# Kernel tuning notes

Hardware: AMD Instinct MI355X
Metric: run time of the kernel (lower is better)

The kernel has to match this reference:

```python
import jax, jax.numpy as jnp
import numpy as np

EMBED = 512
HEADS = 8
HEAD_DIM = EMBED // HEADS


def setup_inputs() -> dict:
    key = jax.random.key(0)
    ks = jax.random.split(key, 12)
    B, L, D = 2, 4096, EMBED
    s = 1.0 / np.sqrt(D)  # torch Linear default init range scale (approx, uniform)
    def lin(k):
        kw, kb = jax.random.split(k)
        W = jax.random.uniform(kw, (D, D), jnp.float32, -s, s)
        b = jax.random.uniform(kb, (D,), jnp.float32, -s, s)
        return W, b
    Wq, bq = lin(ks[0])
    Wk, bk = lin(ks[1])
    Wv, bv = lin(ks[2])
    Wo, bo = lin(ks[3])
    query = jax.random.normal(ks[4], (B, L, D), jnp.float32)
    key_t = jax.random.normal(ks[5], (B, L, D), jnp.float32)
    value = jax.random.normal(ks[6], (B, L, D), jnp.float32)
    return {"query": query, "key": key_t, "value": value,
            "Wq": Wq, "bq": bq, "Wk": Wk, "bk": bk,
            "Wv": Wv, "bv": bv, "Wo": Wo, "bo": bo}


def reference(query, key, value, Wq, bq, Wk, bk, Wv, bv, Wo, bo):
    B, L, D = query.shape
    H, Hd = HEADS, HEAD_DIM
    scale = Hd ** -0.5
    # torch nn.Linear: y = x @ W.T + b
    q = (query @ Wq.T + bq).reshape(B, L, H, Hd).transpose(0, 2, 1, 3)   # [B,H,L,Hd]
    k = (key   @ Wk.T + bk).reshape(B, -1, H, Hd).transpose(0, 2, 1, 3)
    v = (value @ Wv.T + bv).reshape(B, -1, H, Hd).transpose(0, 2, 1, 3)
    scores = jnp.einsum('bhqd,bhkd->bhqk', q, k) * scale                  # [B,H,L,L]
    causal = jnp.triu(jnp.ones((L, L), dtype=bool), k=1)                  # True above diag
    neg = jnp.finfo(scores.dtype).min
    scores = jnp.where(causal, neg, scores)
    attn = jax.nn.softmax(scores, axis=-1)
    # dropout is identity in eval mode
    out = jnp.einsum('bhqk,bhkd->bhqd', attn, v)                          # [B,H,L,Hd]
    out = out.transpose(0, 2, 1, 3).reshape(B, L, D)
    return out @ Wo.T + bo, attn
```

## Files before the change

kernel.cpp:

```cpp
#include <hip/hip_runtime.h>
#include <hip/hip_bf16.h>


typedef __attribute__((ext_vector_type(8))) __bf16 bf16x8;
typedef __attribute__((ext_vector_type(4))) __bf16 bf16v4;
typedef __attribute__((ext_vector_type(4))) float f32x4;

constexpr int LL = 4096;
constexpr int DD = 512;
constexpr int HH = 8;
constexpr int HD = 64;
constexpr int BB = 2;
constexpr int BL = BB * LL;
constexpr size_t OUT_ELEMS = (size_t)BB * LL * DD;
constexpr int CH = 16;
constexpr int NCHUNK = LL / 64 / CH;

static __device__ inline bf16x8 cvt8(const float* p) {
    float4 a = *reinterpret_cast<const float4*>(p);
    float4 b = *reinterpret_cast<const float4*>(p + 4);
    bf16x8 r;
    r[0] = (__bf16)a.x; r[1] = (__bf16)a.y; r[2] = (__bf16)a.z; r[3] = (__bf16)a.w;
    r[4] = (__bf16)b.x; r[5] = (__bf16)b.y; r[6] = (__bf16)b.z; r[7] = (__bf16)b.w;
    return r;
}

__global__ __launch_bounds__(256) void cvt_kernel(
    const float* __restrict__ q, const float* __restrict__ k,
    const float* __restrict__ v, __bf16* __restrict__ o)
{
    constexpr size_t N = (size_t)BL * DD;
    size_t i = ((size_t)blockIdx.x * 256 + threadIdx.x) * 8;
    const float* src = q; size_t j = i;
    if (i >= 2 * N)      { src = v; j = i - 2 * N; }
    else if (i >= N)     { src = k; j = i - N; }
    *reinterpret_cast<bf16x8*>(&o[i]) = cvt8(&src[j]);
}

__global__ __launch_bounds__(256) void qkv_kernel(
    const __bf16* __restrict__ Xb,
    const float* __restrict__ Wq, const float* __restrict__ bq,
    const float* __restrict__ Wk, const float* __restrict__ bk,
    const float* __restrict__ Wv, const float* __restrict__ bv,
    __bf16* __restrict__ Qb, __bf16* __restrict__ Kb, __bf16* __restrict__ Vt)
{
    const int z = blockIdx.z;
    const __bf16* x  = Xb + (size_t)z * BL * DD;
    const float* W   = (z == 0) ? Wq : (z == 1) ? Wk : Wv;
    const float* bia = (z == 0) ? bq : (z == 1) ? bk : bv;

    const int wid = threadIdx.x >> 6;
    const int lane = threadIdx.x & 63;
    const int l15 = lane & 15;
    const int lg  = lane >> 4;

    const int r0 = blockIdx.x * 64;
    const int cb = blockIdx.y;
    const int c0 = cb * 64 + wid * 16;

    f32x4 acc[4] = {};
    for (int k0 = 0; k0 < DD; k0 += 32) {
        bf16x8 bfrag = cvt8(&W[(size_t)(c0 + l15) * DD + k0 + lg * 8]);
#pragma unroll
        for (int mt = 0; mt < 4; ++mt) {
            bf16x8 afrag = *reinterpret_cast<const bf16x8*>(
                &x[(size_t)(r0 + mt * 16 + l15) * DD + k0 + lg * 8]);
            acc[mt] = __builtin_amdgcn_mfma_f32_16x16x32_bf16(afrag, bfrag, acc[mt], 0, 0, 0);
        }
    }

    __shared__ __bf16 T[64][72];
    const float bval = bia[c0 + l15];
#pragma unroll
    for (int mt = 0; mt < 4; ++mt)
#pragma unroll
        for (int i = 0; i < 4; ++i) {
            const float val = acc[mt][i] + bval;
            const int row = mt * 16 + lg * 4 + i;
            const int col = wid * 16 + l15;
            if (z == 2) T[col][row] = (__bf16)val;
            else        T[row][col] = (__bf16)val;
        }
    __syncthreads();

    const int tr  = threadIdx.x >> 2;
    const int seg = threadIdx.x & 3;
    uint4 v0 = *reinterpret_cast<const uint4*>(&T[tr][seg * 16]);
    uint4 v1 = *reinterpret_cast<const uint4*>(&T[tr][seg * 16 + 8]);
    const int b  = r0 >> 12;
    const int l0 = r0 & (LL - 1);
    if (z == 2) {
        __bf16* dst = Vt + ((size_t)(b * HH + cb) * HD + tr) * LL + l0 + seg * 16;
        *reinterpret_cast<uint4*>(dst)     = v0;
        *reinterpret_cast<uint4*>(dst + 8) = v1;
    } else {
        __bf16* base = (z == 0) ? Qb : Kb;
        __bf16* dst = base + ((size_t)(b * HH + cb) * LL + l0 + tr) * HD + seg * 16;
        *reinterpret_cast<uint4*>(dst)     = v0;
        *reinterpret_cast<uint4*>(dst + 8) = v1;
    }
}

__global__ __launch_bounds__(256) void rowsum_kernel(
    const __bf16* __restrict__ Qb, const __bf16* __restrict__ Kb,
    float* __restrict__ rspart)
{
    const int bh = blockIdx.x;
    const int qb = 63 - blockIdx.y;
    const int ch = blockIdx.z;
    if (ch * CH > qb) return;

    const int wv   = threadIdx.x >> 6;
    const int lane = threadIdx.x & 63;
    const int l15  = lane & 15;
    const int lg   = lane >> 4;

    const __bf16* Qh = Qb + (size_t)bh * LL * HD;
    const __bf16* Kh = Kb + (size_t)bh * LL * HD;

    const int q0 = qb * 64 + wv * 16;
    const int qrow = q0 + l15;
    const bf16x8 qf0 = *reinterpret_cast<const bf16x8*>(&Qh[(size_t)qrow * HD + lg * 8]);
    const bf16x8 qf1 = *reinterpret_cast<const bf16x8*>(&Qh[(size_t)qrow * HD + 32 + lg * 8]);
    const float SC = 0.125f * 1.44269504088896f;

    float rs = 0.f;
    const int kend = (qb < ch * CH + CH - 1) ? qb : ch * CH + CH - 1;
    for (int kb = ch * CH; kb <= kend; ++kb) {
        f32x4 s[4] = {};
#pragma unroll
        for (int kt = 0; kt < 4; ++kt) {
            const __bf16* kp = &Kh[(size_t)(kb * 64 + kt * 16 + l15) * HD + lg * 8];
            const bf16x8 k0 = *reinterpret_cast<const bf16x8*>(kp);
            const bf16x8 k1 = *reinterpret_cast<const bf16x8*>(kp + 32);
            s[kt] = __builtin_amdgcn_mfma_f32_16x16x32_bf16(k0, qf0, s[kt], 0, 0, 0);
            s[kt] = __builtin_amdgcn_mfma_f32_16x16x32_bf16(k1, qf1, s[kt], 0, 0, 0);
        }
        const bool diag = (kb == qb);
#pragma unroll
        for (int kt = 0; kt < 4; ++kt)
#pragma unroll
            for (int i = 0; i < 4; ++i) {
                float e = exp2f(s[kt][i] * SC);
                if (diag && (kb * 64 + kt * 16 + lg * 4 + i) > qrow) e = 0.f;
                rs += e;
            }
    }
    rs += __shfl_xor(rs, 16, 64);
    rs += __shfl_xor(rs, 32, 64);
    if (lane < 16)
        rspart[((size_t)bh * LL + qrow) * NCHUNK + ch] = rs;
}

__global__ __launch_bounds__(256, 4) void attn_main_kernel(
    const __bf16* __restrict__ Qb, const __bf16* __restrict__ Kb,
    const __bf16* __restrict__ Vt, const float* __restrict__ rspart,
    __bf16* __restrict__ opart, float* __restrict__ attn_out)
{
    const int bh = blockIdx.x;
    const int qb = 63 - blockIdx.y;
    const int ch = blockIdx.z;

    const int wv   = threadIdx.x >> 6;
    const int lane = threadIdx.x & 63;
    const int l15  = lane & 15;
    const int lg   = lane >> 4;

    float* A_out = attn_out + (size_t)bh * LL * LL;
    const int q0 = qb * 64 + wv * 16;
    const int qrow = q0 + l15;
    const int kb0 = ch * CH;

    if (kb0 > qb) {
        const float4 z4 = {0.f, 0.f, 0.f, 0.f};
        float4* dst = reinterpret_cast<float4*>(&A_out[(size_t)qrow * LL + kb0 * 64 + lg * 4]);
        for (int t = 0; t < CH; ++t) {
#pragma unroll
            for (int kt = 0; kt < 4; ++kt) dst[kt * 4] = z4;
            dst += 16;
        }
        return;
    }

    const __bf16* Qh = Qb + (size_t)bh * LL * HD;
    const __bf16* Kh = Kb + (size_t)bh * LL * HD;
    const __bf16* Vh = Vt + (size_t)bh * HD * LL;

    __shared__ __bf16 P[4][16][72];

    const bf16x8 qf0 = *reinterpret_cast<const bf16x8*>(&Qh[(size_t)qrow * HD + lg * 8]);
    const bf16x8 qf1 = *reinterpret_cast<const bf16x8*>(&Qh[(size_t)qrow * HD + 32 + lg * 8]);

    float rsv = 0.f;
    const int nc = qb >> 4;
    const float* rp = &rspart[((size_t)bh * LL + qrow) * NCHUNK];
    for (int c = 0; c <= nc; ++c) rsv += rp[c];
    const float llog = -log2f(rsv);
    const float SC = 0.125f * 1.44269504088896f;

    f32x4 oacc[4] = {};

    for (int t = 0; t < CH; ++t) {
        const int kb = kb0 + t;
        if (kb > qb) {
            const float4 z4 = {0.f, 0.f, 0.f, 0.f};
            float4* dst = reinterpret_cast<float4*>(
                &A_out[(size_t)qrow * LL + kb * 64 + lg * 4]);
#pragma unroll
            for (int kt = 0; kt < 4; ++kt) dst[kt * 4] = z4;
            continue;
        }
        bf16x8 kf[8], vf[8];
        {
            const __bf16* kp = &Kh[(size_t)(kb * 64 + l15) * HD + lg * 8];
#pragma unroll
            for (int kt = 0; kt < 4; ++kt) {
                kf[kt * 2]     = *reinterpret_cast<const bf16x8*>(kp + (size_t)kt * 16 * HD);
                kf[kt * 2 + 1] = *reinterpret_cast<const bf16x8*>(kp + (size_t)kt * 16 * HD + 32);
            }
            const __bf16* vp = &Vh[(size_t)l15 * LL + (size_t)kb * 64 + lg * 8];
#pragma unroll
            for (int ht = 0; ht < 4; ++ht) {
                vf[ht * 2]     = *reinterpret_cast<const bf16x8*>(vp + (size_t)ht * 16 * LL);
                vf[ht * 2 + 1] = *reinterpret_cast<const bf16x8*>(vp + (size_t)ht * 16 * LL + 32);
            }
        }
        f32x4 s[4] = {};
#pragma unroll
        for (int kt = 0; kt < 4; ++kt) {
            s[kt] = __builtin_amdgcn_mfma_f32_16x16x32_bf16(kf[kt * 2],     qf0, s[kt], 0, 0, 0);
            s[kt] = __builtin_amdgcn_mfma_f32_16x16x32_bf16(kf[kt * 2 + 1], qf1, s[kt], 0, 0, 0);
        }
        const bool diag = (kb == qb);
#pragma unroll
        for (int kt = 0; kt < 4; ++kt) {
            float e0 = exp2f(fmaf(s[kt][0], SC, llog));
            float e1 = exp2f(fmaf(s[kt][1], SC, llog));
            float e2 = exp2f(fmaf(s[kt][2], SC, llog));
            float e3 = exp2f(fmaf(s[kt][3], SC, llog));
            if (diag) {
                const int kc = kb * 64 + kt * 16 + lg * 4;
                if (kc + 0 > qrow) e0 = 0.f;
                if (kc + 1 > qrow) e1 = 0.f;
                if (kc + 2 > qrow) e2 = 0.f;
                if (kc + 3 > qrow) e3 = 0.f;
            }
            float4 ev = {e0, e1, e2, e3};
            *reinterpret_cast<float4*>(
                &A_out[(size_t)qrow * LL + kb * 64 + kt * 16 + lg * 4]) = ev;
            bf16v4 pk;
            pk[0] = (__bf16)e0; pk[1] = (__bf16)e1;
            pk[2] = (__bf16)e2; pk[3] = (__bf16)e3;
            *reinterpret_cast<bf16v4*>(&P[wv][l15][kt * 16 + lg * 4]) = pk;
        }
        const bf16x8 pa0 = *reinterpret_cast<const bf16x8*>(&P[wv][l15][lg * 8]);
        const bf16x8 pa1 = *reinterpret_cast<const bf16x8*>(&P[wv][l15][32 + lg * 8]);
#pragma unroll
        for (int ht = 0; ht < 4; ++ht) {
            oacc[ht] = __builtin_amdgcn_mfma_f32_16x16x32_bf16(pa0, vf[ht * 2],     oacc[ht], 0, 0, 0);
            oacc[ht] = __builtin_amdgcn_mfma_f32_16x16x32_bf16(pa1, vf[ht * 2 + 1], oacc[ht], 0, 0, 0);
        }
    }

#pragma unroll
    for (int ht = 0; ht < 4; ++ht)
#pragma unroll
        for (int i = 0; i < 4; ++i)
            P[wv][lg * 4 + i][ht * 16 + l15] = (__bf16)oacc[ht][i];
    const int arow = lane >> 2;
    const int aseg = lane & 3;
    uint4 o0 = *reinterpret_cast<const uint4*>(&P[wv][arow][aseg * 16]);
    uint4 o1 = *reinterpret_cast<const uint4*>(&P[wv][arow][aseg * 16 + 8]);
    __bf16* dst = opart + ((size_t)((bh * 64 + qb) * NCHUNK + ch)) * 4096
                + (wv * 16 + arow) * 64 + aseg * 16;
    *reinterpret_cast<uint4*>(dst)     = o0;
    *reinterpret_cast<uint4*>(dst + 8) = o1;
}

__global__ __launch_bounds__(256) void oreduce_kernel(
    const __bf16* __restrict__ opart, __bf16* __restrict__ Ob)
{
    const int bh = blockIdx.x;
    const int qb = blockIdx.y;
    const int nc = qb >> 4;
    const __bf16* src = opart + ((size_t)(bh * 64 + qb) * NCHUNK) * 4096;
    const int t = threadIdx.x;

    float acc[16] = {};
    for (int c = 0; c <= nc; ++c) {
        bf16x8 a = *reinterpret_cast<const bf16x8*>(&src[(size_t)c * 4096 + t * 16]);
        bf16x8 b = *reinterpret_cast<const bf16x8*>(&src[(size_t)c * 4096 + t * 16 + 8]);
#pragma unroll
        for (int j = 0; j < 8; ++j) { acc[j] += (float)a[j]; acc[8 + j] += (float)b[j]; }
    }
    bf16x8 r0, r1;
#pragma unroll
    for (int j = 0; j < 8; ++j) { r0[j] = (__bf16)acc[j]; r1[j] = (__bf16)acc[8 + j]; }

    const int qr  = t >> 2;
    const int hd0 = (t & 3) * 16;
    const int b = bh >> 3, h = bh & 7;
    __bf16* dst = Ob + ((size_t)(b * LL + qb * 64 + qr)) * DD + h * HD + hd0;
    *reinterpret_cast<bf16x8*>(dst)     = r0;
    *reinterpret_cast<bf16x8*>(dst + 8) = r1;
}

__global__ __launch_bounds__(256) void oproj_kernel(
    const __bf16* __restrict__ Ob, const float* __restrict__ Wo,
    const float* __restrict__ bo, float* __restrict__ out)
{
    const int wid = threadIdx.x >> 6;
    const int lane = threadIdx.x & 63;
    const int l15 = lane & 15;
    const int lg  = lane >> 4;

    const int r0 = blockIdx.x * 64;
    const int c0 = blockIdx.y * 64 + wid * 16;

    f32x4 acc[4] = {};
    for (int k0 = 0; k0 < DD; k0 += 32) {
        bf16x8 bfrag = cvt8(&Wo[(size_t)(c0 + l15) * DD + k0 + lg * 8]);
#pragma unroll
        for (int mt = 0; mt < 4; ++mt) {
            bf16x8 afrag = *reinterpret_cast<const bf16x8*>(
                &Ob[(size_t)(r0 + mt * 16 + l15) * DD + k0 + lg * 8]);
            acc[mt] = __builtin_amdgcn_mfma_f32_16x16x32_bf16(afrag, bfrag, acc[mt], 0, 0, 0);
        }
    }
    const float bval = bo[c0 + l15];
#pragma unroll
    for (int mt = 0; mt < 4; ++mt)
#pragma unroll
        for (int i = 0; i < 4; ++i)
            out[(size_t)(r0 + mt * 16 + lg * 4 + i) * DD + c0 + l15] = acc[mt][i] + bval;
}

extern "C" void kernel_launch(void* const* d_in, const int* in_sizes, int n_in,
                              void* d_out, int out_size, void* d_ws, size_t ws_size,
                              hipStream_t stream) {
    const float* query = (const float*)d_in[0];
    const float* key_t = (const float*)d_in[1];
    const float* value = (const float*)d_in[2];
    const float* Wq = (const float*)d_in[3];
    const float* bq = (const float*)d_in[4];
    const float* Wk = (const float*)d_in[5];
    const float* bk = (const float*)d_in[6];
    const float* Wv = (const float*)d_in[7];
    const float* bv = (const float*)d_in[8];
    const float* Wo = (const float*)d_in[9];
    const float* bo = (const float*)d_in[10];

    float* out  = (float*)d_out;
    float* attn = out + OUT_ELEMS;

    char* ws = (char*)d_ws;
    __bf16* Qb     = (__bf16*)(ws);
    __bf16* Kb     = (__bf16*)(ws +  8388608);
    __bf16* Vt     = (__bf16*)(ws + 16777216);
    __bf16* Ob     = (__bf16*)(ws + 25165824);
    float*  rspart = (float*) (ws + 33554432);
    __bf16* Xb     = (__bf16*)(ws + 34603008);
    __bf16* opart  = (__bf16*)(ws + 34603008);

    cvt_kernel<<<dim3(3 * BL * DD / 8 / 256), 256, 0, stream>>>(query, key_t, value, Xb);
    qkv_kernel<<<dim3(BL / 64, DD / 64, 3), 256, 0, stream>>>(
        Xb, Wq, bq, Wk, bk, Wv, bv, Qb, Kb, Vt);
    rowsum_kernel<<<dim3(BB * HH, LL / 64, NCHUNK), 256, 0, stream>>>(Qb, Kb, rspart);
    attn_main_kernel<<<dim3(BB * HH, LL / 64, NCHUNK), 256, 0, stream>>>(
        Qb, Kb, Vt, rspart, opart, attn);
    oreduce_kernel<<<dim3(BB * HH, LL / 64), 256, 0, stream>>>(opart, Ob);
    oproj_kernel<<<dim3(BL / 64, DD / 64), 256, 0, stream>>>(Ob, Wo, bo, out);
}
```

Baseline: 786.8 us.

## Stage attention probs through LDS for coalesced nontemporal stores and double-buffer K loads

The attention-probability tile is now staged through an fp32 shared buffer so each wave writes full contiguous 256-byte row segments with nontemporal stores, replacing the scattered column-fragment stores. K fragments are double-buffered in registers across key blocks in both rowsum and main kernels. The grid is reordered so chunks vary fastest, and the launch bounds change (main kernel drops to 3 waves per SIMD target). The extra LDS buffer and register pressure from double buffering may lower occupancy.

```diff
diff --git a/kernel.cpp b/kernel.cpp
--- a/kernel.cpp
+++ b/kernel.cpp
@@ -101,13 +101,13 @@
     }
 }
 
-__global__ __launch_bounds__(256) void rowsum_kernel(
+__global__ __launch_bounds__(256, 4) void rowsum_kernel(
     const __bf16* __restrict__ Qb, const __bf16* __restrict__ Kb,
     float* __restrict__ rspart)
 {
-    const int bh = blockIdx.x;
+    const int ch = blockIdx.x;
     const int qb = 63 - blockIdx.y;
-    const int ch = blockIdx.z;
+    const int bh = blockIdx.z;
     if (ch * CH > qb) return;
 
     const int wv   = threadIdx.x >> 6;
@@ -124,17 +124,22 @@
     const bf16x8 qf1 = *reinterpret_cast<const bf16x8*>(&Qh[(size_t)qrow * HD + 32 + lg * 8]);
     const float SC = 0.125f * 1.44269504088896f;
 
+    auto loadK = [&](bf16x8 (&kf)[8], int kb) {
+        const __bf16* kp = &Kh[((size_t)kb * 64 + l15) * HD + lg * 8];
+#pragma unroll
+        for (int kt = 0; kt < 4; ++kt) {
+            kf[kt * 2]     = *reinterpret_cast<const bf16x8*>(kp + (size_t)kt * 16 * HD);
+            kf[kt * 2 + 1] = *reinterpret_cast<const bf16x8*>(kp + (size_t)kt * 16 * HD + 32);
+        }
+    };
+
     float rs = 0.f;
-    const int kend = (qb < ch * CH + CH - 1) ? qb : ch * CH + CH - 1;
-    for (int kb = ch * CH; kb <= kend; ++kb) {
+    auto body = [&](bf16x8 (&kf)[8], int kb) {
         f32x4 s[4] = {};
 #pragma unroll
         for (int kt = 0; kt < 4; ++kt) {
-            const __bf16* kp = &Kh[(size_t)(kb * 64 + kt * 16 + l15) * HD + lg * 8];
-            const bf16x8 k0 = *reinterpret_cast<const bf16x8*>(kp);
-            const bf16x8 k1 = *reinterpret_cast<const bf16x8*>(kp + 32);
-            s[kt] = __builtin_amdgcn_mfma_f32_16x16x32_bf16(k0, qf0, s[kt], 0, 0, 0);
-            s[kt] = __builtin_amdgcn_mfma_f32_16x16x32_bf16(k1, qf1, s[kt], 0, 0, 0);
+            s[kt] = __builtin_amdgcn_mfma_f32_16x16x32_bf16(kf[kt * 2],     qf0, s[kt], 0, 0, 0);
+            s[kt] = __builtin_amdgcn_mfma_f32_16x16x32_bf16(kf[kt * 2 + 1], qf1, s[kt], 0, 0, 0);
         }
         const bool diag = (kb == qb);
 #pragma unroll
@@ -145,6 +150,19 @@
                 if (diag && (kb * 64 + kt * 16 + lg * 4 + i) > qrow) e = 0.f;
                 rs += e;
             }
+    };
+
+    const int kend = (qb < ch * CH + CH - 1) ? qb : ch * CH + CH - 1;
+    {
+        bf16x8 kA[8], kB[8];
+        int kb = ch * CH;
+        bool useA = true;
+        loadK(kA, kb);
+        for (; kb <= kend; ++kb) {
+            if (useA) { if (kb + 1 <= kend) loadK(kB, kb + 1); body(kA, kb); }
+            else      { if (kb + 1 <= kend) loadK(kA, kb + 1); body(kB, kb); }
+            useA = !useA;
+        }
     }
     rs += __shfl_xor(rs, 16, 64);
     rs += __shfl_xor(rs, 32, 64);
@@ -152,14 +170,14 @@
         rspart[((size_t)bh * LL + qrow) * NCHUNK + ch] = rs;
 }
 
-__global__ __launch_bounds__(256, 4) void attn_main_kernel(
+__global__ __launch_bounds__(256, 3) void attn_main_kernel(
     const __bf16* __restrict__ Qb, const __bf16* __restrict__ Kb,
     const __bf16* __restrict__ Vt, const float* __restrict__ rspart,
     __bf16* __restrict__ opart, float* __restrict__ attn_out)
 {
-    const int bh = blockIdx.x;
+    const int ch = blockIdx.x;
     const int qb = 63 - blockIdx.y;
-    const int ch = blockIdx.z;
+    const int bh = blockIdx.z;
 
     const int wv   = threadIdx.x >> 6;
     const int lane = threadIdx.x & 63;
@@ -171,14 +189,19 @@
     const int qrow = q0 + l15;
     const int kb0 = ch * CH;
 
+    const int srow = lane >> 4;
+    const int scol = (lane & 15) * 4;
+
+    auto zstore = [&](int kb) {
+        const f32x4 z4 = {0.f, 0.f, 0.f, 0.f};
+#pragma unroll
+        for (int mt = 0; mt < 4; ++mt)
+            __builtin_nontemporal_store(z4, reinterpret_cast<f32x4*>(
+                &A_out[(size_t)(q0 + mt * 4 + srow) * LL + kb * 64 + scol]));
+    };
+
     if (kb0 > qb) {
-        const float4 z4 = {0.f, 0.f, 0.f, 0.f};
-        float4* dst = reinterpret_cast<float4*>(&A_out[(size_t)qrow * LL + kb0 * 64 + lg * 4]);
-        for (int t = 0; t < CH; ++t) {
-#pragma unroll
-            for (int kt = 0; kt < 4; ++kt) dst[kt * 4] = z4;
-            dst += 16;
-        }
+        for (int t = 0; t < CH; ++t) zstore(kb0 + t);
         return;
     }
 
@@ -186,7 +209,8 @@
     const __bf16* Kh = Kb + (size_t)bh * LL * HD;
     const __bf16* Vh = Vt + (size_t)bh * HD * LL;
 
-    __shared__ __bf16 P[4][16][72];
+    __shared__ float  Pf[4][16][68];
+    __shared__ __bf16 Pb[4][16][72];
 
     const bf16x8 qf0 = *reinterpret_cast<const bf16x8*>(&Qh[(size_t)qrow * HD + lg * 8]);
     const bf16x8 qf1 = *reinterpret_cast<const bf16x8*>(&Qh[(size_t)qrow * HD + 32 + lg * 8]);
@@ -200,24 +224,18 @@
 
     f32x4 oacc[4] = {};
 
-    for (int t = 0; t < CH; ++t) {
-        const int kb = kb0 + t;
-        if (kb > qb) {
-            const float4 z4 = {0.f, 0.f, 0.f, 0.f};
-            float4* dst = reinterpret_cast<float4*>(
-                &A_out[(size_t)qrow * LL + kb * 64 + lg * 4]);
-#pragma unroll
-            for (int kt = 0; kt < 4; ++kt) dst[kt * 4] = z4;
-            continue;
-        }
-        bf16x8 kf[8], vf[8];
+    auto loadK = [&](bf16x8 (&kf)[8], int kb) {
+        const __bf16* kp = &Kh[((size_t)kb * 64 + l15) * HD + lg * 8];
+#pragma unroll
+        for (int kt = 0; kt < 4; ++kt) {
+            kf[kt * 2]     = *reinterpret_cast<const bf16x8*>(kp + (size_t)kt * 16 * HD);
+            kf[kt * 2 + 1] = *reinterpret_cast<const bf16x8*>(kp + (size_t)kt * 16 * HD + 32);
+        }
+    };
+
+    auto body = [&](bf16x8 (&kf)[8], int kb) {
+        bf16x8 vf[8];
         {
-            const __bf16* kp = &Kh[(size_t)(kb * 64 + l15) * HD + lg * 8];
-#pragma unroll
-            for (int kt = 0; kt < 4; ++kt) {
-                kf[kt * 2]     = *reinterpret_cast<const bf16x8*>(kp + (size_t)kt * 16 * HD);
-                kf[kt * 2 + 1] = *reinterpret_cast<const bf16x8*>(kp + (size_t)kt * 16 * HD + 32);
-            }
             const __bf16* vp = &Vh[(size_t)l15 * LL + (size_t)kb * 64 + lg * 8];
 #pragma unroll
             for (int ht = 0; ht < 4; ++ht) {
@@ -245,32 +263,51 @@
                 if (kc + 2 > qrow) e2 = 0.f;
                 if (kc + 3 > qrow) e3 = 0.f;
             }
-            float4 ev = {e0, e1, e2, e3};
-            *reinterpret_cast<float4*>(
-                &A_out[(size_t)qrow * LL + kb * 64 + kt * 16 + lg * 4]) = ev;
+            f32x4 ev = {e0, e1, e2, e3};
+            *reinterpret_cast<f32x4*>(&Pf[wv][l15][kt * 16 + lg * 4]) = ev;
             bf16v4 pk;
             pk[0] = (__bf16)e0; pk[1] = (__bf16)e1;
             pk[2] = (__bf16)e2; pk[3] = (__bf16)e3;
-            *reinterpret_cast<bf16v4*>(&P[wv][l15][kt * 16 + lg * 4]) = pk;
-        }
-        const bf16x8 pa0 = *reinterpret_cast<const bf16x8*>(&P[wv][l15][lg * 8]);
-        const bf16x8 pa1 = *reinterpret_cast<const bf16x8*>(&P[wv][l15][32 + lg * 8]);
+            *reinterpret_cast<bf16v4*>(&Pb[wv][l15][kt * 16 + lg * 4]) = pk;
+        }
+#pragma unroll
+        for (int mt = 0; mt < 4; ++mt) {
+            f32x4 v = *reinterpret_cast<const f32x4*>(&Pf[wv][mt * 4 + srow][scol]);
+            __builtin_nontemporal_store(v, reinterpret_cast<f32x4*>(
+                &A_out[(size_t)(q0 + mt * 4 + srow) * LL + kb * 64 + scol]));
+        }
+        const bf16x8 pa0 = *reinterpret_cast<const bf16x8*>(&Pb[wv][l15][lg * 8]);
+        const bf16x8 pa1 = *reinterpret_cast<const bf16x8*>(&Pb[wv][l15][32 + lg * 8]);
 #pragma unroll
         for (int ht = 0; ht < 4; ++ht) {
             oacc[ht] = __builtin_amdgcn_mfma_f32_16x16x32_bf16(pa0, vf[ht * 2],     oacc[ht], 0, 0, 0);
             oacc[ht] = __builtin_amdgcn_mfma_f32_16x16x32_bf16(pa1, vf[ht * 2 + 1], oacc[ht], 0, 0, 0);
         }
-    }
+    };
+
+    const int kend = (qb < kb0 + CH - 1) ? qb : kb0 + CH - 1;
+    {
+        bf16x8 kA[8], kB[8];
+        int kb = kb0;
+        bool useA = true;
+        loadK(kA, kb);
+        for (; kb <= kend; ++kb) {
+            if (useA) { if (kb + 1 <= kend) loadK(kB, kb + 1); body(kA, kb); }
+            else      { if (kb + 1 <= kend) loadK(kA, kb + 1); body(kB, kb); }
+            useA = !useA;
+        }
+    }
+    for (int kb = qb + 1; kb < kb0 + CH; ++kb) zstore(kb);
 
 #pragma unroll
     for (int ht = 0; ht < 4; ++ht)
 #pragma unroll
         for (int i = 0; i < 4; ++i)
-            P[wv][lg * 4 + i][ht * 16 + l15] = (__bf16)oacc[ht][i];
+            Pb[wv][lg * 4 + i][ht * 16 + l15] = (__bf16)oacc[ht][i];
     const int arow = lane >> 2;
     const int aseg = lane & 3;
-    uint4 o0 = *reinterpret_cast<const uint4*>(&P[wv][arow][aseg * 16]);
-    uint4 o1 = *reinterpret_cast<const uint4*>(&P[wv][arow][aseg * 16 + 8]);
+    uint4 o0 = *reinterpret_cast<const uint4*>(&Pb[wv][arow][aseg * 16]);
+    uint4 o1 = *reinterpret_cast<const uint4*>(&Pb[wv][arow][aseg * 16 + 8]);
     __bf16* dst = opart + ((size_t)((bh * 64 + qb) * NCHUNK + ch)) * 4096
                 + (wv * 16 + arow) * 64 + aseg * 16;
     *reinterpret_cast<uint4*>(dst)     = o0;
@@ -365,8 +402,8 @@
     cvt_kernel<<<dim3(3 * BL * DD / 8 / 256), 256, 0, stream>>>(query, key_t, value, Xb);
     qkv_kernel<<<dim3(BL / 64, DD / 64, 3), 256, 0, stream>>>(
         Xb, Wq, bq, Wk, bk, Wv, bv, Qb, Kb, Vt);
-    rowsum_kernel<<<dim3(BB * HH, LL / 64, NCHUNK), 256, 0, stream>>>(Qb, Kb, rspart);
-    attn_main_kernel<<<dim3(BB * HH, LL / 64, NCHUNK), 256, 0, stream>>>(
+    rowsum_kernel<<<dim3(NCHUNK, LL / 64, BB * HH), 256, 0, stream>>>(Qb, Kb, rspart);
+    attn_main_kernel<<<dim3(NCHUNK, LL / 64, BB * HH), 256, 0, stream>>>(
         Qb, Kb, Vt, rspart, opart, attn);
     oreduce_kernel<<<dim3(BB * HH, LL / 64), 256, 0, stream>>>(opart, Ob);
     oproj_kernel<<<dim3(BL / 64, DD / 64), 256, 0, stream>>>(Ob, Wo, bo, out);
```

After: 1.008 ms. 1.28x slower.

## Fuse rowsum, attention and output reduction into one per-query-block kernel

Applied to the files above, without the earlier changes.

Replaces the three-kernel attention path (chunked row-sum pass, chunked main pass writing partial outputs, and a reduction kernel) with one kernel per (batch-head, query block). Each block computes the softmax denominator over all keys itself, then does the probability and PV pass and writes O directly. This removes the rspart and opart workspace traffic and two launches. In exchange it drops the key-chunk split, so there are only 1024 blocks of very uneven length, which reduces parallelism and load balance. The upper-triangle zero fill is now done by each block at the start.

```diff
diff --git a/kernel.cpp b/kernel.cpp
--- a/kernel.cpp
+++ b/kernel.cpp
@@ -13,8 +13,6 @@
 constexpr int BB = 2;
 constexpr int BL = BB * LL;
 constexpr size_t OUT_ELEMS = (size_t)BB * LL * DD;
-constexpr int CH = 16;
-constexpr int NCHUNK = LL / 64 / CH;
 
 static __device__ inline bf16x8 cvt8(const float* p) {
     float4 a = *reinterpret_cast<const float4*>(p);
@@ -101,38 +99,52 @@
     }
 }
 
-__global__ __launch_bounds__(256) void rowsum_kernel(
+__global__ __launch_bounds__(256) void attn_fused_kernel(
     const __bf16* __restrict__ Qb, const __bf16* __restrict__ Kb,
-    float* __restrict__ rspart)
+    const __bf16* __restrict__ Vt, __bf16* __restrict__ Ob,
+    float* __restrict__ attn_out)
 {
     const int bh = blockIdx.x;
     const int qb = 63 - blockIdx.y;
-    const int ch = blockIdx.z;
-    if (ch * CH > qb) return;
 
     const int wv   = threadIdx.x >> 6;
     const int lane = threadIdx.x & 63;
     const int l15  = lane & 15;
     const int lg   = lane >> 4;
 
+    float* A_out = attn_out + (size_t)bh * LL * LL;
+    const int q0 = qb * 64 + wv * 16;
+    const int qrow = q0 + l15;
+
+    {
+        const f32x4 z4 = {0.f, 0.f, 0.f, 0.f};
+        const int c0 = (qb + 1) * 64;
+#pragma unroll 1
+        for (int r = 0; r < 16; ++r) {
+            float* row = A_out + (size_t)(q0 + r) * LL;
+            for (int c = c0 + lane * 4; c < LL; c += 256)
+                *reinterpret_cast<f32x4*>(row + c) = z4;
+        }
+    }
+
     const __bf16* Qh = Qb + (size_t)bh * LL * HD;
     const __bf16* Kh = Kb + (size_t)bh * LL * HD;
-
-    const int q0 = qb * 64 + wv * 16;
-    const int qrow = q0 + l15;
+    const __bf16* Vh = Vt + (size_t)bh * HD * LL;
+
+    __shared__ __bf16 P[4][16][72];
+
     const bf16x8 qf0 = *reinterpret_cast<const bf16x8*>(&Qh[(size_t)qrow * HD + lg * 8]);
     const bf16x8 qf1 = *reinterpret_cast<const bf16x8*>(&Qh[(size_t)qrow * HD + 32 + lg * 8]);
     const float SC = 0.125f * 1.44269504088896f;
 
     float rs = 0.f;
-    const int kend = (qb < ch * CH + CH - 1) ? qb : ch * CH + CH - 1;
-    for (int kb = ch * CH; kb <= kend; ++kb) {
+    for (int kb = 0; kb <= qb; ++kb) {
+        const __bf16* kp = &Kh[((size_t)kb * 64 + l15) * HD + lg * 8];
         f32x4 s[4] = {};
 #pragma unroll
         for (int kt = 0; kt < 4; ++kt) {
-            const __bf16* kp = &Kh[(size_t)(kb * 64 + kt * 16 + l15) * HD + lg * 8];
-            const bf16x8 k0 = *reinterpret_cast<const bf16x8*>(kp);
-            const bf16x8 k1 = *reinterpret_cast<const bf16x8*>(kp + 32);
+            bf16x8 k0 = *reinterpret_cast<const bf16x8*>(kp + (size_t)kt * 16 * HD);
+            bf16x8 k1 = *reinterpret_cast<const bf16x8*>(kp + (size_t)kt * 16 * HD + 32);
             s[kt] = __builtin_amdgcn_mfma_f32_16x16x32_bf16(k0, qf0, s[kt], 0, 0, 0);
             s[kt] = __builtin_amdgcn_mfma_f32_16x16x32_bf16(k1, qf1, s[kt], 0, 0, 0);
         }
@@ -148,88 +160,28 @@
     }
     rs += __shfl_xor(rs, 16, 64);
     rs += __shfl_xor(rs, 32, 64);
-    if (lane < 16)
-        rspart[((size_t)bh * LL + qrow) * NCHUNK + ch] = rs;
-}
-
-__global__ __launch_bounds__(256, 4) void attn_main_kernel(
-    const __bf16* __restrict__ Qb, const __bf16* __restrict__ Kb,
-    const __bf16* __restrict__ Vt, const float* __restrict__ rspart,
-    __bf16* __restrict__ opart, float* __restrict__ attn_out)
-{
-    const int bh = blockIdx.x;
-    const int qb = 63 - blockIdx.y;
-    const int ch = blockIdx.z;
-
-    const int wv   = threadIdx.x >> 6;
-    const int lane = threadIdx.x & 63;
-    const int l15  = lane & 15;
-    const int lg   = lane >> 4;
-
-    float* A_out = attn_out + (size_t)bh * LL * LL;
-    const int q0 = qb * 64 + wv * 16;
-    const int qrow = q0 + l15;
-    const int kb0 = ch * CH;
-
-    if (kb0 > qb) {
-        const float4 z4 = {0.f, 0.f, 0.f, 0.f};
-        float4* dst = reinterpret_cast<float4*>(&A_out[(size_t)qrow * LL + kb0 * 64 + lg * 4]);
-        for (int t = 0; t < CH; ++t) {
-#pragma unroll
-            for (int kt = 0; kt < 4; ++kt) dst[kt * 4] = z4;
-            dst += 16;
-        }
-        return;
-    }
-
-    const __bf16* Qh = Qb + (size_t)bh * LL * HD;
-    const __bf16* Kh = Kb + (size_t)bh * LL * HD;
-    const __bf16* Vh = Vt + (size_t)bh * HD * LL;
-
-    __shared__ __bf16 P[4][16][72];
-
-    const bf16x8 qf0 = *reinterpret_cast<const bf16x8*>(&Qh[(size_t)qrow * HD + lg * 8]);
-    const bf16x8 qf1 = *reinterpret_cast<const bf16x8*>(&Qh[(size_t)qrow * HD + 32 + lg * 8]);
-
-    float rsv = 0.f;
-    const int nc = qb >> 4;
-    const float* rp = &rspart[((size_t)bh * LL + qrow) * NCHUNK];
-    for (int c = 0; c <= nc; ++c) rsv += rp[c];
-    const float llog = -log2f(rsv);
-    const float SC = 0.125f * 1.44269504088896f;
+    const float llog = -log2f(rs);
 
     f32x4 oacc[4] = {};
-
-    for (int t = 0; t < CH; ++t) {
-        const int kb = kb0 + t;
-        if (kb > qb) {
-            const float4 z4 = {0.f, 0.f, 0.f, 0.f};
-            float4* dst = reinterpret_cast<float4*>(
-                &A_out[(size_t)qrow * LL + kb * 64 + lg * 4]);
-#pragma unroll
-            for (int kt = 0; kt < 4; ++kt) dst[kt * 4] = z4;
-            continue;
-        }
-        bf16x8 kf[8], vf[8];
-        {
-            const __bf16* kp = &Kh[(size_t)(kb * 64 + l15) * HD + lg * 8];
-#pragma unroll
-            for (int kt = 0; kt < 4; ++kt) {
-                kf[kt * 2]     = *reinterpret_cast<const bf16x8*>(kp + (size_t)kt * 16 * HD);
-                kf[kt * 2 + 1] = *reinterpret_cast<const bf16x8*>(kp + (size_t)kt * 16 * HD + 32);
-            }
-            const __bf16* vp = &Vh[(size_t)l15 * LL + (size_t)kb * 64 + lg * 8];
-#pragma unroll
-            for (int ht = 0; ht < 4; ++ht) {
-                vf[ht * 2]     = *reinterpret_cast<const bf16x8*>(vp + (size_t)ht * 16 * LL);
-                vf[ht * 2 + 1] = *reinterpret_cast<const bf16x8*>(vp + (size_t)ht * 16 * LL + 32);
-            }
-        }
+    for (int kb = 0; kb <= qb; ++kb) {
+        const __bf16* kp = &Kh[((size_t)kb * 64 + l15) * HD + lg * 8];
+        const __bf16* vp = &Vh[(size_t)l15 * LL + (size_t)kb * 64 + lg * 8];
+        bf16x8 vf0 = *reinterpret_cast<const bf16x8*>(vp + (size_t)0 * 16 * LL);
+        bf16x8 vf1 = *reinterpret_cast<const bf16x8*>(vp + (size_t)0 * 16 * LL + 32);
+        bf16x8 vf2 = *reinterpret_cast<const bf16x8*>(vp + (size_t)1 * 16 * LL);
+        bf16x8 vf3 = *reinterpret_cast<const bf16x8*>(vp + (size_t)1 * 16 * LL + 32);
+        bf16x8 vf4 = *reinterpret_cast<const bf16x8*>(vp + (size_t)2 * 16 * LL);
+        bf16x8 vf5 = *reinterpret_cast<const bf16x8*>(vp + (size_t)2 * 16 * LL + 32);
+        bf16x8 vf6 = *reinterpret_cast<const bf16x8*>(vp + (size_t)3 * 16 * LL);
+        bf16x8 vf7 = *reinterpret_cast<const bf16x8*>(vp + (size_t)3 * 16 * LL + 32);
+
         f32x4 s[4] = {};
 #pragma unroll
         for (int kt = 0; kt < 4; ++kt) {
-            s[kt] = __builtin_amdgcn_mfma_f32_16x16x32_bf16(kf[kt * 2],     qf0, s[kt], 0, 0, 0);
-            s[kt] = __builtin_amdgcn_mfma_f32_16x16x32_bf16(kf[kt * 2 + 1], qf1, s[kt], 0, 0, 0);
+            bf16x8 k0 = *reinterpret_cast<const bf16x8*>(kp + (size_t)kt * 16 * HD);
+            bf16x8 k1 = *reinterpret_cast<const bf16x8*>(kp + (size_t)kt * 16 * HD + 32);
+            s[kt] = __builtin_amdgcn_mfma_f32_16x16x32_bf16(k0, qf0, s[kt], 0, 0, 0);
+            s[kt] = __builtin_amdgcn_mfma_f32_16x16x32_bf16(k1, qf1, s[kt], 0, 0, 0);
         }
         const bool diag = (kb == qb);
 #pragma unroll
@@ -245,8 +197,8 @@
                 if (kc + 2 > qrow) e2 = 0.f;
                 if (kc + 3 > qrow) e3 = 0.f;
             }
-            float4 ev = {e0, e1, e2, e3};
-            *reinterpret_cast<float4*>(
+            f32x4 ev = {e0, e1, e2, e3};
+            *reinterpret_cast<f32x4*>(
                 &A_out[(size_t)qrow * LL + kb * 64 + kt * 16 + lg * 4]) = ev;
             bf16v4 pk;
             pk[0] = (__bf16)e0; pk[1] = (__bf16)e1;
@@ -255,11 +207,14 @@
         }
         const bf16x8 pa0 = *reinterpret_cast<const bf16x8*>(&P[wv][l15][lg * 8]);
         const bf16x8 pa1 = *reinterpret_cast<const bf16x8*>(&P[wv][l15][32 + lg * 8]);
-#pragma unroll
-        for (int ht = 0; ht < 4; ++ht) {
-            oacc[ht] = __builtin_amdgcn_mfma_f32_16x16x32_bf16(pa0, vf[ht * 2],     oacc[ht], 0, 0, 0);
-            oacc[ht] = __builtin_amdgcn_mfma_f32_16x16x32_bf16(pa1, vf[ht * 2 + 1], oacc[ht], 0, 0, 0);
-        }
+        oacc[0] = __builtin_amdgcn_mfma_f32_16x16x32_bf16(pa0, vf0, oacc[0], 0, 0, 0);
+        oacc[0] = __builtin_amdgcn_mfma_f32_16x16x32_bf16(pa1, vf1, oacc[0], 0, 0, 0);
+        oacc[1] = __builtin_amdgcn_mfma_f32_16x16x32_bf16(pa0, vf2, oacc[1], 0, 0, 0);
+        oacc[1] = __builtin_amdgcn_mfma_f32_16x16x32_bf16(pa1, vf3, oacc[1], 0, 0, 0);
+        oacc[2] = __builtin_amdgcn_mfma_f32_16x16x32_bf16(pa0, vf4, oacc[2], 0, 0, 0);
+        oacc[2] = __builtin_amdgcn_mfma_f32_16x16x32_bf16(pa1, vf5, oacc[2], 0, 0, 0);
+        oacc[3] = __builtin_amdgcn_mfma_f32_16x16x32_bf16(pa0, vf6, oacc[3], 0, 0, 0);
+        oacc[3] = __builtin_amdgcn_mfma_f32_16x16x32_bf16(pa1, vf7, oacc[3], 0, 0, 0);
     }
 
 #pragma unroll
@@ -271,38 +226,10 @@
     const int aseg = lane & 3;
     uint4 o0 = *reinterpret_cast<const uint4*>(&P[wv][arow][aseg * 16]);
     uint4 o1 = *reinterpret_cast<const uint4*>(&P[wv][arow][aseg * 16 + 8]);
-    __bf16* dst = opart + ((size_t)((bh * 64 + qb) * NCHUNK + ch)) * 4096
-                + (wv * 16 + arow) * 64 + aseg * 16;
+    const int b = bh >> 3, h = bh & 7;
+    __bf16* dst = Ob + ((size_t)(b * LL + q0 + arow)) * DD + h * HD + aseg * 16;
     *reinterpret_cast<uint4*>(dst)     = o0;
     *reinterpret_cast<uint4*>(dst + 8) = o1;
-}
-
-__global__ __launch_bounds__(256) void oreduce_kernel(
-    const __bf16* __restrict__ opart, __bf16* __restrict__ Ob)
-{
-    const int bh = blockIdx.x;
-    const int qb = blockIdx.y;
-    const int nc = qb >> 4;
-    const __bf16* src = opart + ((size_t)(bh * 64 + qb) * NCHUNK) * 4096;
-    const int t = threadIdx.x;
-
-    float acc[16] = {};
-    for (int c = 0; c <= nc; ++c) {
-        bf16x8 a = *reinterpret_cast<const bf16x8*>(&src[(size_t)c * 4096 + t * 16]);
-        bf16x8 b = *reinterpret_cast<const bf16x8*>(&src[(size_t)c * 4096 + t * 16 + 8]);
-#pragma unroll
-        for (int j = 0; j < 8; ++j) { acc[j] += (float)a[j]; acc[8 + j] += (float)b[j]; }
-    }
-    bf16x8 r0, r1;
-#pragma unroll
-    for (int j = 0; j < 8; ++j) { r0[j] = (__bf16)acc[j]; r1[j] = (__bf16)acc[8 + j]; }
-
-    const int qr  = t >> 2;
-    const int hd0 = (t & 3) * 16;
-    const int b = bh >> 3, h = bh & 7;
-    __bf16* dst = Ob + ((size_t)(b * LL + qb * 64 + qr)) * DD + h * HD + hd0;
-    *reinterpret_cast<bf16x8*>(dst)     = r0;
-    *reinterpret_cast<bf16x8*>(dst + 8) = r1;
 }
 
 __global__ __launch_bounds__(256) void oproj_kernel(
@@ -354,20 +281,15 @@
     float* attn = out + OUT_ELEMS;
 
     char* ws = (char*)d_ws;
-    __bf16* Qb     = (__bf16*)(ws);
-    __bf16* Kb     = (__bf16*)(ws +  8388608);
-    __bf16* Vt     = (__bf16*)(ws + 16777216);
-    __bf16* Ob     = (__bf16*)(ws + 25165824);
-    float*  rspart = (float*) (ws + 33554432);
-    __bf16* Xb     = (__bf16*)(ws + 34603008);
-    __bf16* opart  = (__bf16*)(ws + 34603008);
+    __bf16* Qb = (__bf16*)(ws);
+    __bf16* Kb = (__bf16*)(ws +  8388608);
+    __bf16* Vt = (__bf16*)(ws + 16777216);
+    __bf16* Ob = (__bf16*)(ws + 25165824);
+    __bf16* Xb = (__bf16*)(ws + 33554432);
 
     cvt_kernel<<<dim3(3 * BL * DD / 8 / 256), 256, 0, stream>>>(query, key_t, value, Xb);
     qkv_kernel<<<dim3(BL / 64, DD / 64, 3), 256, 0, stream>>>(
         Xb, Wq, bq, Wk, bk, Wv, bv, Qb, Kb, Vt);
-    rowsum_kernel<<<dim3(BB * HH, LL / 64, NCHUNK), 256, 0, stream>>>(Qb, Kb, rspart);
-    attn_main_kernel<<<dim3(BB * HH, LL / 64, NCHUNK), 256, 0, stream>>>(
-        Qb, Kb, Vt, rspart, opart, attn);
-    oreduce_kernel<<<dim3(BB * HH, LL / 64), 256, 0, stream>>>(opart, Ob);
+    attn_fused_kernel<<<dim3(BB * HH, LL / 64), 256, 0, stream>>>(Qb, Kb, Vt, Ob, attn);
     oproj_kernel<<<dim3(BL / 64, DD / 64), 256, 0, stream>>>(Ob, Wo, bo, out);
 }
```

Result: faster. 736.1 us (median of 2 runs) (-6.5%).
